# Kernel optimization log

Measured on AMD Instinct MI355X. Metric: run time of the kernel, lower is better.

Reference implementation:

```python
import jax, jax.numpy as jnp
import numpy as np

IOU_THR = 0.8
SCORE_THR = 0.7
INNER_THR = 0.5
EPS = 1e-8


def setup_inputs() -> dict:
    key = jax.random.key(0)
    k1, k2 = jax.random.split(key)
    N, H, W = 1024, 256, 256
    masks = (jax.random.uniform(k1, (N, H, W)) < 0.15).astype(jnp.float32)
    scores = jax.random.uniform(k2, (N,), dtype=jnp.float32)
    return {"masks": masks, "scores": scores}


def reference(masks, scores):
    N = masks.shape[0]
    # sort by score descending (torch: scores.sort(0, descending=True))
    order = jnp.argsort(-scores)
    s = scores[order]
    flat = masks[order].reshape(N, -1).astype(jnp.float32)  # [N, H*W]
    area = jnp.sum(flat, axis=1)                            # [N]

    inter = flat @ flat.T                                   # [N, N]
    union = area[None, :] + area[:, None] - inter
    iou = inter / (union + EPS)
    ratio_i = inter / (area[:, None] + EPS)
    ratio_j = inter / (area[None, :] + EPS)
    vals = 1.0 - ratio_j * ratio_i

    cond1 = (ratio_i < 0.5) & (ratio_j >= 0.85)
    cond2 = (ratio_i >= 0.85) & (ratio_j < 0.5)
    # inner_iou_matrix[cond1] = vals[cond1]
    inner = jnp.where(cond1, vals, 0.0)
    # inner_iou_matrix.T[cond2] = vals[cond2]  =>  inner[j,i] = vals[i,j] where cond2[i,j]
    inner = jnp.where(cond2.T, vals.T, inner)

    triu1 = jnp.triu(jnp.ones((N, N), dtype=bool), k=1)
    tril1 = jnp.tril(jnp.ones((N, N), dtype=bool), k=1)  # note diagonal=1, matches torch.tril(., 1)

    iou_max = jnp.max(jnp.where(triu1, iou, 0.0), axis=0)
    inner_max_u = jnp.max(jnp.where(triu1, inner, 0.0), axis=0)
    inner_max_l = jnp.max(jnp.where(tril1, inner, 0.0), axis=0)

    keep = iou_max <= IOU_THR
    keep_conf = s > SCORE_THR
    # fallback: if no mask passes score threshold, keep top-3 by score
    _, top3 = jax.lax.top_k(s, 3)
    fallback = jnp.zeros((N,), dtype=bool).at[top3].set(True)
    keep_conf = jnp.where(jnp.any(keep_conf), keep_conf, fallback)

    keep = keep & keep_conf & (inner_max_u <= 1.0 - INNER_THR) & (inner_max_l <= 1.0 - INNER_THR)
    # torch returns idx[keep] (dynamic shape); we return (order, keep) which is equivalent info
    return order, keep
```

## Files before the change

kernel.cpp:

```cpp
#include <hip/hip_runtime.h>


#define N_MASKS 1024
#define HW 65536
#define WPR 2048
#define NT 16
#define NPAIRS 136
#define KQ 4

__device__ __forceinline__ void tile_from_pair(int p, int& I, int& J) {
    int rem = p, i = 0;
    while (rem >= NT - i) { rem -= NT - i; ++i; }
    I = i; J = i + rem;
}

__global__ __launch_bounds__(128) void sort_kernel(const float* __restrict__ scores,
                                                   int* __restrict__ order,
                                                   float* __restrict__ ssort,
                                                   int* __restrict__ out_order,
                                                   float* __restrict__ area,
                                                   unsigned* __restrict__ ioumax,
                                                   unsigned* __restrict__ innu,
                                                   unsigned* __restrict__ innl) {
    __shared__ float s[N_MASKS];
    const int t = threadIdx.x;
    for (int k = t; k < N_MASKS; k += 128) s[k] = scores[k];
    __syncthreads();
    const int i = blockIdx.x * 128 + t;
    const float si = s[i];
    int rank = 0;
    #pragma unroll 8
    for (int j = 0; j < N_MASKS; ++j) {
        const float sj = s[j];
        rank += (int)((sj > si) || (sj == si && j < i));
    }
    order[rank] = i;
    ssort[rank] = si;
    out_order[rank] = i;
    area[i] = 0.0f;
    ioumax[i] = 0u; innu[i] = 0u; innl[i] = 0u;
}

__global__ __launch_bounds__(256) void pack_kernel(const float* __restrict__ masks,
                                                   const int* __restrict__ order,
                                                   unsigned* __restrict__ packed,
                                                   float* __restrict__ area) {
    const int b = blockIdx.x;
    const int r = b >> 1, half = b & 1;
    const int src = order[r];
    const float4* __restrict__ row = (const float4*)(masks + (size_t)src * HW) + half * 8192;
    unsigned* __restrict__ prow = packed + (size_t)r * WPR + half * 1024;
    const int t = threadIdx.x;
    int cnt = 0;
    #pragma unroll
    for (int g = 0; g < 4; ++g) {
        unsigned bits = 0u;
        #pragma unroll
        for (int k = 0; k < 8; ++k) {
            const float4 f = row[g * 2048 + k * 256 + t];
            unsigned nib = (unsigned)(f.x != 0.0f)
                         | ((unsigned)(f.y != 0.0f) << 1)
                         | ((unsigned)(f.z != 0.0f) << 2)
                         | ((unsigned)(f.w != 0.0f) << 3);
            bits |= nib << (k * 4);
        }
        prow[g * 256 + t] = bits;
        cnt += __builtin_popcount(bits);
    }
    for (int off = 32; off > 0; off >>= 1) cnt += __shfl_down(cnt, off, 64);
    __shared__ int red[4];
    const int lane = t & 63, w = t >> 6;
    if (lane == 0) red[w] = cnt;
    __syncthreads();
    if (t == 0) atomicAdd(area + r, (float)(red[0] + red[1] + red[2] + red[3]));
}

__global__ __launch_bounds__(256, 2) void pair_kernel(const unsigned* __restrict__ packed,
                                                      unsigned* __restrict__ partial) {
    __shared__ __align__(16) unsigned lA[64 * 64];
    __shared__ __align__(16) unsigned lB[64 * 64];

    const int p = blockIdx.x, kq = blockIdx.y;
    int I, J; tile_from_pair(p, I, J);
    const int A0 = I * 64, B0 = J * 64;
    const int t = threadIdx.x;
    const int tx = t & 15, ty = t >> 4;

    unsigned acc[4][4] = {};

    const int c0 = kq * (WPR / 64 / KQ);
    for (int c = c0; c < c0 + (WPR / 64 / KQ); ++c) {
        __syncthreads();
        #pragma unroll
        for (int rep = 0; rep < 4; ++rep) {
            const int linear = rep * 1024 + t * 4;
            const int row = linear >> 6, col = linear & 63;
            const int phys = row * 64 + (((col >> 2) ^ (row >> 2)) << 2);
            const uint4 va = *(const uint4*)(packed + (size_t)(A0 + row) * WPR + c * 64 + col);
            const uint4 vb = *(const uint4*)(packed + (size_t)(B0 + row) * WPR + c * 64 + col);
            *(uint4*)(lA + phys) = va;
            *(uint4*)(lB + phys) = vb;
        }
        __syncthreads();
        #pragma unroll
        for (int g = 0; g < 16; ++g) {
            uint4 a[4], b[4];
            #pragma unroll
            for (int i = 0; i < 4; ++i)
                a[i] = *(const uint4*)(lA + (ty * 4 + i) * 64 + ((g ^ ty) << 2));
            #pragma unroll
            for (int j = 0; j < 4; ++j)
                b[j] = *(const uint4*)(lB + (tx * 4 + j) * 64 + ((g ^ tx) << 2));
            #pragma unroll
            for (int i = 0; i < 4; ++i)
                #pragma unroll
                for (int j = 0; j < 4; ++j) {
                    acc[i][j] += __builtin_popcount(a[i].x & b[j].x);
                    acc[i][j] += __builtin_popcount(a[i].y & b[j].y);
                    acc[i][j] += __builtin_popcount(a[i].z & b[j].z);
                    acc[i][j] += __builtin_popcount(a[i].w & b[j].w);
                }
        }
    }

    unsigned* __restrict__ out = partial + ((size_t)kq * NPAIRS + p) * 4096;
    #pragma unroll
    for (int i = 0; i < 4; ++i) {
        uint4 v = make_uint4(acc[i][0], acc[i][1], acc[i][2], acc[i][3]);
        *(uint4*)(out + (ty * 4 + i) * 64 + tx * 4) = v;
    }
}

__global__ __launch_bounds__(256) void combine_kernel(const unsigned* __restrict__ partial,
                                                      const float* __restrict__ area,
                                                      unsigned* __restrict__ ioumax,
                                                      unsigned* __restrict__ innu,
                                                      unsigned* __restrict__ innl) {
    __shared__ float aA[64], aB[64];
    __shared__ unsigned redI[64], redU[64], redLA[64], redLB[64];

    const int p = blockIdx.x;
    int I, J; tile_from_pair(p, I, J);
    const int A0 = I * 64, B0 = J * 64;
    const int t = threadIdx.x;
    if (t < 64) {
        aA[t] = area[A0 + t]; aB[t] = area[B0 + t];
        redI[t] = 0u; redU[t] = 0u; redLA[t] = 0u; redLB[t] = 0u;
    }
    __syncthreads();

    const int tx = t & 15, ty = t >> 4;
    float mI[4] = {0,0,0,0}, mU[4] = {0,0,0,0}, mLB[4] = {0,0,0,0}, mLA[4] = {0,0,0,0};

    #pragma unroll
    for (int i = 0; i < 4; ++i) {
        const int arow = ty * 4 + i;
        const int a = A0 + arow;
        const size_t off = (size_t)p * 4096 + arow * 64 + tx * 4;
        const uint4 s0 = *(const uint4*)(partial + 0u * NPAIRS * 4096 + off);
        const uint4 s1 = *(const uint4*)(partial + 1u * NPAIRS * 4096 + off);
        const uint4 s2 = *(const uint4*)(partial + 2u * NPAIRS * 4096 + off);
        const uint4 s3 = *(const uint4*)(partial + 3u * NPAIRS * 4096 + off);
        unsigned sums[4] = { s0.x + s1.x + s2.x + s3.x, s0.y + s1.y + s2.y + s3.y,
                             s0.z + s1.z + s2.z + s3.z, s0.w + s1.w + s2.w + s3.w };
        const float fa = aA[arow];
        #pragma unroll
        for (int j = 0; j < 4; ++j) {
            const int b = B0 + tx * 4 + j;
            if (a > b) continue;
            const float inter = (float)sums[j];
            const float fb = aB[tx * 4 + j];
            const float uni = (fb + fa) - inter;
            const float iou = inter / (uni + 1e-8f);
            const float ra = inter / (fa + 1e-8f);
            const float rb = inter / (fb + 1e-8f);
            const float v = __fsub_rn(1.0f, __fmul_rn(rb, ra));
            const float iab = (ra < 0.5f && rb >= 0.85f) ? v : 0.0f;
            const float iba = (rb < 0.5f && ra >= 0.85f) ? v : 0.0f;
            if (a < b) {
                mI[j] = fmaxf(mI[j], iou);
                mU[j] = fmaxf(mU[j], iab);
                mLA[i] = fmaxf(mLA[i], iba);
            }
            if (a == b - 1) mLB[j] = fmaxf(mLB[j], iab);
        }
    }
    #pragma unroll
    for (int j = 0; j < 4; ++j) {
        atomicMax(&redI[tx * 4 + j], __float_as_uint(mI[j]));
        atomicMax(&redU[tx * 4 + j], __float_as_uint(mU[j]));
        atomicMax(&redLB[tx * 4 + j], __float_as_uint(mLB[j]));
    }
    #pragma unroll
    for (int i = 0; i < 4; ++i)
        atomicMax(&redLA[ty * 4 + i], __float_as_uint(mLA[i]));
    __syncthreads();
    if (t < 64) {
        atomicMax(&ioumax[B0 + t], redI[t]);
        atomicMax(&innu[B0 + t], redU[t]);
        atomicMax(&innl[B0 + t], redLB[t]);
        atomicMax(&innl[A0 + t], redLA[t]);
    }
}

__global__ __launch_bounds__(256) void keep_kernel(const float* __restrict__ ssort,
                                                   const unsigned* __restrict__ ioumax,
                                                   const unsigned* __restrict__ innu,
                                                   const unsigned* __restrict__ innl,
                                                   int* __restrict__ out_keep) {
    const int r = blockIdx.x * 256 + threadIdx.x;
    const float s0 = ssort[0];
    const bool conf = (s0 > 0.7f) ? (ssort[r] > 0.7f) : (r < 3);
    const bool keep = (__uint_as_float(ioumax[r]) <= 0.8f) && conf &&
                      (__uint_as_float(innu[r]) <= 0.5f) &&
                      (__uint_as_float(innl[r]) <= 0.5f);
    out_keep[r] = keep ? 1 : 0;
}

extern "C" void kernel_launch(void* const* d_in, const int* in_sizes, int n_in,
                              void* d_out, int out_size, void* d_ws, size_t ws_size,
                              hipStream_t stream) {
    const float* masks  = (const float*)d_in[0];
    const float* scores = (const float*)d_in[1];
    int* out = (int*)d_out;

    unsigned* packed  = (unsigned*)d_ws;
    unsigned* partial = packed + (size_t)N_MASKS * WPR;
    unsigned* tail    = partial + (size_t)KQ * NPAIRS * 4096;
    int*      order   = (int*)tail;
    float*    ssort   = (float*)(order + N_MASKS);
    float*    area    = (float*)(ssort + N_MASKS);
    unsigned* ioumax  = (unsigned*)(area + N_MASKS);
    unsigned* innu    = ioumax + N_MASKS;
    unsigned* innl    = innu + N_MASKS;

    sort_kernel<<<8, 128, 0, stream>>>(scores, order, ssort, out, area, ioumax, innu, innl);
    pack_kernel<<<2048, 256, 0, stream>>>(masks, order, packed, area);
    pair_kernel<<<dim3(NPAIRS, KQ), 256, 0, stream>>>(packed, partial);
    combine_kernel<<<NPAIRS, 256, 0, stream>>>(partial, area, ioumax, innu, innl);
    keep_kernel<<<4, 256, 0, stream>>>(ssort, ioumax, innu, innl, out + N_MASKS);
}
```

Baseline: 503.3 us.

## Enlarge pair tiles to 128x128 with 8x8 register blocking and wider K split

Doubles the popcount-GEMM tile from 64x64 to 128x128 rows, with each thread accumulating an 8x8 block, and splits K into 16 slices instead of 4. This cuts LDS reads per popcount and reduces blocks spent on diagonal tiles. The combine kernel is restructured to sum the 16 partial slices over row groups. It adds register pressure and a larger partial-sum buffer to write and read back.

```diff
diff --git a/kernel.cpp b/kernel.cpp
--- a/kernel.cpp
+++ b/kernel.cpp
@@ -4,9 +4,9 @@
 #define N_MASKS 1024
 #define HW 65536
 #define WPR 2048
-#define NT 16
-#define NPAIRS 136
-#define KQ 4
+#define NT 8
+#define NPAIRS 36
+#define KQ 16
 
 __device__ __forceinline__ void tile_from_pair(int p, int& I, int& J) {
     int rem = p, i = 0;
@@ -77,44 +77,44 @@
 
 __global__ __launch_bounds__(256, 2) void pair_kernel(const unsigned* __restrict__ packed,
                                                       unsigned* __restrict__ partial) {
-    __shared__ __align__(16) unsigned lA[64 * 64];
-    __shared__ __align__(16) unsigned lB[64 * 64];
+    __shared__ __align__(16) unsigned lA[128 * 64];
+    __shared__ __align__(16) unsigned lB[128 * 64];
 
     const int p = blockIdx.x, kq = blockIdx.y;
     int I, J; tile_from_pair(p, I, J);
-    const int A0 = I * 64, B0 = J * 64;
+    const int A0 = I * 128, B0 = J * 128;
     const int t = threadIdx.x;
     const int tx = t & 15, ty = t >> 4;
 
-    unsigned acc[4][4] = {};
-
-    const int c0 = kq * (WPR / 64 / KQ);
-    for (int c = c0; c < c0 + (WPR / 64 / KQ); ++c) {
+    unsigned acc[8][8] = {};
+
+    const int c0 = kq * 2;
+    for (int c = c0; c < c0 + 2; ++c) {
         __syncthreads();
         #pragma unroll
-        for (int rep = 0; rep < 4; ++rep) {
-            const int linear = rep * 1024 + t * 4;
-            const int row = linear >> 6, col = linear & 63;
-            const int phys = row * 64 + (((col >> 2) ^ (row >> 2)) << 2);
-            const uint4 va = *(const uint4*)(packed + (size_t)(A0 + row) * WPR + c * 64 + col);
-            const uint4 vb = *(const uint4*)(packed + (size_t)(B0 + row) * WPR + c * 64 + col);
+        for (int it = 0; it < 8; ++it) {
+            const int linear = it * 256 + t;
+            const int row = linear >> 4, c16 = linear & 15;
+            const int phys = row * 64 + ((c16 ^ (row >> 3)) << 2);
+            const uint4 va = *(const uint4*)(packed + (size_t)(A0 + row) * WPR + c * 64 + c16 * 4);
+            const uint4 vb = *(const uint4*)(packed + (size_t)(B0 + row) * WPR + c * 64 + c16 * 4);
             *(uint4*)(lA + phys) = va;
             *(uint4*)(lB + phys) = vb;
         }
         __syncthreads();
         #pragma unroll
         for (int g = 0; g < 16; ++g) {
-            uint4 a[4], b[4];
+            uint4 a[8], b[8];
             #pragma unroll
-            for (int i = 0; i < 4; ++i)
-                a[i] = *(const uint4*)(lA + (ty * 4 + i) * 64 + ((g ^ ty) << 2));
+            for (int i = 0; i < 8; ++i)
+                a[i] = *(const uint4*)(lA + (ty * 8 + i) * 64 + ((g ^ ty) << 2));
             #pragma unroll
-            for (int j = 0; j < 4; ++j)
-                b[j] = *(const uint4*)(lB + (tx * 4 + j) * 64 + ((g ^ tx) << 2));
+            for (int j = 0; j < 8; ++j)
+                b[j] = *(const uint4*)(lB + (tx * 8 + j) * 64 + ((g ^ tx) << 2));
             #pragma unroll
-            for (int i = 0; i < 4; ++i)
+            for (int i = 0; i < 8; ++i)
                 #pragma unroll
-                for (int j = 0; j < 4; ++j) {
+                for (int j = 0; j < 8; ++j) {
                     acc[i][j] += __builtin_popcount(a[i].x & b[j].x);
                     acc[i][j] += __builtin_popcount(a[i].y & b[j].y);
                     acc[i][j] += __builtin_popcount(a[i].z & b[j].z);
@@ -123,11 +123,13 @@
         }
     }
 
-    unsigned* __restrict__ out = partial + ((size_t)kq * NPAIRS + p) * 4096;
-    #pragma unroll
-    for (int i = 0; i < 4; ++i) {
-        uint4 v = make_uint4(acc[i][0], acc[i][1], acc[i][2], acc[i][3]);
-        *(uint4*)(out + (ty * 4 + i) * 64 + tx * 4) = v;
+    unsigned* __restrict__ out = partial + ((size_t)kq * NPAIRS + p) * (128 * 128);
+    #pragma unroll
+    for (int i = 0; i < 8; ++i) {
+        uint4 v0 = make_uint4(acc[i][0], acc[i][1], acc[i][2], acc[i][3]);
+        uint4 v1 = make_uint4(acc[i][4], acc[i][5], acc[i][6], acc[i][7]);
+        *(uint4*)(out + (ty * 8 + i) * 128 + tx * 8) = v0;
+        *(uint4*)(out + (ty * 8 + i) * 128 + tx * 8 + 4) = v1;
     }
 }
 
@@ -136,71 +138,59 @@
                                                       unsigned* __restrict__ ioumax,
                                                       unsigned* __restrict__ innu,
                                                       unsigned* __restrict__ innl) {
-    __shared__ float aA[64], aB[64];
-    __shared__ unsigned redI[64], redU[64], redLA[64], redLB[64];
-
-    const int p = blockIdx.x;
+    __shared__ unsigned redI[128], redU[128], redLB[128], redLA[8];
+    __shared__ float aB[128];
+
+    const int p = blockIdx.x, rg = blockIdx.y;
     int I, J; tile_from_pair(p, I, J);
-    const int A0 = I * 64, B0 = J * 64;
-    const int t = threadIdx.x;
-    if (t < 64) {
-        aA[t] = area[A0 + t]; aB[t] = area[B0 + t];
-        redI[t] = 0u; redU[t] = 0u; redLA[t] = 0u; redLB[t] = 0u;
-    }
-    __syncthreads();
-
-    const int tx = t & 15, ty = t >> 4;
-    float mI[4] = {0,0,0,0}, mU[4] = {0,0,0,0}, mLB[4] = {0,0,0,0}, mLA[4] = {0,0,0,0};
-
-    #pragma unroll
-    for (int i = 0; i < 4; ++i) {
-        const int arow = ty * 4 + i;
-        const int a = A0 + arow;
-        const size_t off = (size_t)p * 4096 + arow * 64 + tx * 4;
-        const uint4 s0 = *(const uint4*)(partial + 0u * NPAIRS * 4096 + off);
-        const uint4 s1 = *(const uint4*)(partial + 1u * NPAIRS * 4096 + off);
-        const uint4 s2 = *(const uint4*)(partial + 2u * NPAIRS * 4096 + off);
-        const uint4 s3 = *(const uint4*)(partial + 3u * NPAIRS * 4096 + off);
-        unsigned sums[4] = { s0.x + s1.x + s2.x + s3.x, s0.y + s1.y + s2.y + s3.y,
-                             s0.z + s1.z + s2.z + s3.z, s0.w + s1.w + s2.w + s3.w };
-        const float fa = aA[arow];
-        #pragma unroll
-        for (int j = 0; j < 4; ++j) {
-            const int b = B0 + tx * 4 + j;
-            if (a > b) continue;
-            const float inter = (float)sums[j];
-            const float fb = aB[tx * 4 + j];
-            const float uni = (fb + fa) - inter;
-            const float iou = inter / (uni + 1e-8f);
-            const float ra = inter / (fa + 1e-8f);
-            const float rb = inter / (fb + 1e-8f);
-            const float v = __fsub_rn(1.0f, __fmul_rn(rb, ra));
-            const float iab = (ra < 0.5f && rb >= 0.85f) ? v : 0.0f;
-            const float iba = (rb < 0.5f && ra >= 0.85f) ? v : 0.0f;
-            if (a < b) {
-                mI[j] = fmaxf(mI[j], iou);
-                mU[j] = fmaxf(mU[j], iab);
-                mLA[i] = fmaxf(mLA[i], iba);
-            }
-            if (a == b - 1) mLB[j] = fmaxf(mLB[j], iab);
-        }
-    }
+    const int A0 = I * 128, B0 = J * 128;
+    const int t = threadIdx.x;
+    if (t < 128) { redI[t] = 0u; redU[t] = 0u; redLB[t] = 0u; aB[t] = area[B0 + t]; }
+    if (t < 8) redLA[t] = 0u;
+    __syncthreads();
+
+    const int row = rg * 8 + (t >> 5);
+    const int col = (t & 31) * 4;
+    const int a = A0 + row;
+    const float fa = area[a];
+
+    unsigned sx = 0, sy = 0, sz = 0, sw = 0;
+    #pragma unroll
+    for (int kq = 0; kq < KQ; ++kq) {
+        const uint4 v = *(const uint4*)(partial + ((size_t)kq * NPAIRS + p) * 16384 + row * 128 + col);
+        sx += v.x; sy += v.y; sz += v.z; sw += v.w;
+    }
+    const unsigned sums[4] = { sx, sy, sz, sw };
+
+    float mLA = 0.0f;
     #pragma unroll
     for (int j = 0; j < 4; ++j) {
-        atomicMax(&redI[tx * 4 + j], __float_as_uint(mI[j]));
-        atomicMax(&redU[tx * 4 + j], __float_as_uint(mU[j]));
-        atomicMax(&redLB[tx * 4 + j], __float_as_uint(mLB[j]));
-    }
-    #pragma unroll
-    for (int i = 0; i < 4; ++i)
-        atomicMax(&redLA[ty * 4 + i], __float_as_uint(mLA[i]));
-    __syncthreads();
-    if (t < 64) {
+        const int b = B0 + col + j;
+        if (a > b) continue;
+        const float inter = (float)sums[j];
+        const float fb = aB[col + j];
+        const float uni = (fb + fa) - inter;
+        const float iou = inter / (uni + 1e-8f);
+        const float ra = inter / (fa + 1e-8f);
+        const float rb = inter / (fb + 1e-8f);
+        const float v = __fsub_rn(1.0f, __fmul_rn(rb, ra));
+        const float iab = (ra < 0.5f && rb >= 0.85f) ? v : 0.0f;
+        const float iba = (rb < 0.5f && ra >= 0.85f) ? v : 0.0f;
+        if (a < b) {
+            atomicMax(&redI[col + j], __float_as_uint(iou));
+            atomicMax(&redU[col + j], __float_as_uint(iab));
+            mLA = fmaxf(mLA, iba);
+        }
+        if (a == b - 1) atomicMax(&redLB[col + j], __float_as_uint(iab));
+    }
+    atomicMax(&redLA[t >> 5], __float_as_uint(mLA));
+    __syncthreads();
+    if (t < 128) {
         atomicMax(&ioumax[B0 + t], redI[t]);
         atomicMax(&innu[B0 + t], redU[t]);
         atomicMax(&innl[B0 + t], redLB[t]);
-        atomicMax(&innl[A0 + t], redLA[t]);
-    }
+    }
+    if (t < 8) atomicMax(&innl[A0 + rg * 8 + t], redLA[t]);
 }
 
 __global__ __launch_bounds__(256) void keep_kernel(const float* __restrict__ ssort,
@@ -226,7 +216,7 @@
 
     unsigned* packed  = (unsigned*)d_ws;
     unsigned* partial = packed + (size_t)N_MASKS * WPR;
-    unsigned* tail    = partial + (size_t)KQ * NPAIRS * 4096;
+    unsigned* tail    = partial + (size_t)KQ * NPAIRS * 16384;
     int*      order   = (int*)tail;
     float*    ssort   = (float*)(order + N_MASKS);
     float*    area    = (float*)(ssort + N_MASKS);
@@ -237,6 +227,6 @@
     sort_kernel<<<8, 128, 0, stream>>>(scores, order, ssort, out, area, ioumax, innu, innl);
     pack_kernel<<<2048, 256, 0, stream>>>(masks, order, packed, area);
     pair_kernel<<<dim3(NPAIRS, KQ), 256, 0, stream>>>(packed, partial);
-    combine_kernel<<<NPAIRS, 256, 0, stream>>>(partial, area, ioumax, innu, innl);
+    combine_kernel<<<dim3(NPAIRS, 16), 256, 0, stream>>>(partial, area, ioumax, innu, innl);
     keep_kernel<<<4, 256, 0, stream>>>(ssort, ioumax, innu, innl, out + N_MASKS);
 }
```

After: 606.5 us. +20.5%, slower.
